# Performance work log

Measured on AMD Instinct MI355X. Metric: run time of the kernel, lower is better.

Reference implementation:

```python
import jax, jax.numpy as jnp
import numpy as np

EPS = float(np.finfo(np.float32).eps)  # matches torch.finfo(float32).eps
N_PTS, K_DIM, N_BINS = 1_000_000, 3, 21  # wv_tilde last dim = 2*N_BINS+1 = 43


def setup_inputs() -> dict:
    key = jax.random.key(0)
    k1, k2 = jax.random.split(key)
    # y in the open unit interval (points on the unit hypercube, per-coordinate)
    y = jax.random.uniform(k1, (N_PTS, K_DIM), jnp.float32, 1e-4, 1.0 - 1e-4)
    # network-predicted unnormalized widths/heights: [N, k, 2b+1]
    wv_tilde = jax.random.normal(k2, (N_PTS, K_DIM, 2 * N_BINS + 1), jnp.float32)
    return {"y": y, "wv_tilde": wv_tilde}


def _gather(t, idx):
    # gather along last axis with [..., 1] int index -> [...]
    return jnp.take_along_axis(t, idx, axis=-1)[..., 0]


def pwquad_flow(y, wv_tilde):
    """Faithful JAX port of ElementWisePWQuadraticTransform.flow (with jacobian)."""
    D = wv_tilde.shape[-1]
    nv = (D + 1) // 2                      # ceil(D/2) = b+1 vertex heights
    v_tilde = wv_tilde[..., :nv]           # [N,k,b+1]
    w_tilde = wv_tilde[..., nv:]           # [N,k,b]
    b = w_tilde.shape[-1]

    # normalized bin widths and their cumulative sums
    w = jnp.exp(w_tilde)
    wsum = jnp.cumsum(w, axis=-1)
    wnorm = wsum[..., -1:]
    w = w / wnorm
    wsum = wsum / wnorm
    zeros = jnp.zeros(wsum.shape[:-1] + (1,), wsum.dtype)
    wsum_shift = jnp.concatenate([zeros, wsum], axis=-1)   # [N,k,b+1]

    # modified softmax for vertex heights of the derivative (integrates to 1)
    ve = jnp.exp(v_tilde)
    trap = (ve[..., :-1] + ve[..., 1:]) * 0.5 * w          # trapezoid areas
    v = jnp.maximum(ve / trap.sum(-1, keepdims=True), 1e-6)  # [N,k,b+1]

    # cumulative CDF values at bin edges
    vw = jnp.concatenate(
        [zeros, jnp.cumsum((v[..., :-1] + v[..., 1:]) * 0.5 * w, axis=-1)],
        axis=-1)                                           # [N,k,b+1]

    # argmax-based bin search (identical to torch implementation)
    finder = jnp.where(vw > y[..., None], 0.0, 1.0)
    cat = jnp.concatenate([jnp.full_like(zeros, EPS), finder * (vw + 1.0)], axis=-1)
    mx = jnp.argmax(cat, axis=-1) - 1
    edges = jnp.clip(mx, 0, b - 1).astype(jnp.int32)[..., None]  # [N,k,1]

    v0 = _gather(v, edges)
    v1 = _gather(v, edges + 1)
    we = _gather(w, edges)

    # quadratic solve: (a/2) t^2 + bq t + c = 0  within the bin
    a = (v1 - v0) * we
    bq = v0 * we
    c = _gather(vw, edges) - y
    a = jnp.where(jnp.abs(a) < EPS, EPS, a)
    d = jnp.maximum(bq * bq - 2.0 * a * c, 0.0)
    sq = jnp.sqrt(d)
    sol1 = (-bq - sq) / a
    sol2 = (-bq + sq) / a
    sol = jnp.where((sol1 >= 0.0) & (sol1 < 1.0), sol1, sol2)
    sol = jnp.clip(sol, EPS, 1.0 - EPS)

    x = we * sol + _gather(wsum_shift, edges)
    x = jnp.clip(x, EPS, 1.0 - EPS)

    # log|det J| = -sum log(lerp(v0, v1, sol))
    logj = -jnp.sum(jnp.log(v0 + (v1 - v0) * sol), axis=-1, keepdims=True)
    return x, logj


def reference(y, wv_tilde):
    return pwquad_flow(y, wv_tilde)
```

## Files before the change

kernel.cpp:

```cpp
#include <hip/hip_runtime.h>
#include <math.h>

#define NROWS        3000000
#define ROWS_PER_BLK 192
#define NBINS        21
#define NV           22
#define DROW         43
#define FLOATS_PER_BLK (ROWS_PER_BLK * DROW)
#define F4_PER_BLK     (FLOATS_PER_BLK / 4)

__global__ __launch_bounds__(ROWS_PER_BLK) void pwquad_kernel(
    const float* __restrict__ y,
    const float* __restrict__ wv,
    float* __restrict__ out)
{
    __shared__ float lds[FLOATS_PER_BLK];
    __shared__ float lt[ROWS_PER_BLK];

    const int tid = threadIdx.x;
    const int blk = blockIdx.x;

    const float4* __restrict__ src4 =
        reinterpret_cast<const float4*>(wv + (long long)blk * FLOATS_PER_BLK);
    float4* l4 = reinterpret_cast<float4*>(lds);

    float4 r[10];
#pragma unroll
    for (int it = 0; it < 10; ++it) r[it] = src4[tid + it * ROWS_PER_BLK];
    const bool tail = (tid < (F4_PER_BLK - 10 * ROWS_PER_BLK));
    float4 rt;
    if (tail) rt = src4[tid + 10 * ROWS_PER_BLK];
#pragma unroll
    for (int it = 0; it < 10; ++it) l4[tid + it * ROWS_PER_BLK] = r[it];
    if (tail) l4[tid + 10 * ROWS_PER_BLK] = rt;
    __syncthreads();

    const int row = blk * ROWS_PER_BLK + tid;
    const float yv = y[row];
    const float* myrow = lds + tid * DROW;

    const float EPSF = 1.1920929e-07f;

    float w[NBINS];
    float wnorm = 0.f;
#pragma unroll
    for (int j = 0; j < NBINS; ++j) { w[j] = __expf(myrow[NV + j]); wnorm += w[j]; }
    const float invw = 1.0f / wnorm;
#pragma unroll
    for (int j = 0; j < NBINS; ++j) w[j] *= invw;

    float v[NV];
#pragma unroll
    for (int i = 0; i < NV; ++i) v[i] = __expf(myrow[i]);
    float T = 0.f;
#pragma unroll
    for (int j = 0; j < NBINS; ++j) T += (v[j] + v[j + 1]) * 0.5f * w[j];
    const float invT = 1.0f / T;
#pragma unroll
    for (int i = 0; i < NV; ++i) v[i] = fmaxf(v[i] * invT, 1e-6f);

    float vw = 0.f, wsum = 0.f;
    float vwe = 0.f, wse = 0.f;
    float v0 = v[0], v1 = v[1], we = w[0];
#pragma unroll
    for (int j = 0; j < 20; ++j) {
        const float inc = (v[j] + v[j + 1]) * 0.5f * w[j];
        vw += inc;
        wsum += w[j];
        const bool q = (vw <= yv);
        vwe = q ? vw       : vwe;
        wse = q ? wsum     : wse;
        v0  = q ? v[j + 1] : v0;
        v1  = q ? v[j + 2] : v1;
        we  = q ? w[j + 1] : we;
    }

    float a = (v1 - v0) * we;
    const float bq = v0 * we;
    const float c = vwe - yv;
    a = (fabsf(a) < EPSF) ? EPSF : a;
    const float dd = fmaxf(bq * bq - 2.0f * a * c, 0.f);
    const float sq = sqrtf(dd);
    const float sol1 = (-bq - sq) / a;
    const float sol2 = (-bq + sq) / a;
    float sol = (sol1 >= 0.f && sol1 < 1.f) ? sol1 : sol2;
    sol = fminf(fmaxf(sol, EPSF), 1.f - EPSF);
    float x = we * sol + wse;
    x = fminf(fmaxf(x, EPSF), 1.f - EPSF);
    out[row] = x;

    lt[tid] = __logf(v0 + (v1 - v0) * sol);
    __syncthreads();
    if (tid % 3 == 0) {
        out[NROWS + blk * (ROWS_PER_BLK / 3) + tid / 3] =
            -(lt[tid] + lt[tid + 1] + lt[tid + 2]);
    }
}

extern "C" void kernel_launch(void* const* d_in, const int* in_sizes, int n_in,
                              void* d_out, int out_size, void* d_ws, size_t ws_size,
                              hipStream_t stream) {
    const float* y  = (const float*)d_in[0];
    const float* wv = (const float*)d_in[1];
    float* out = (float*)d_out;

    const int nblocks = NROWS / ROWS_PER_BLK;
    pwquad_kernel<<<nblocks, ROWS_PER_BLK, 0, stream>>>(y, wv, out);
}
```

Baseline: 98.47 us.

## Load rows directly from global into registers, drop LDS staging and barriers

Replaces block-wide cooperative LDS staging of the 43-float rows with per-thread direct global loads of eleven unaligned 4-wide vectors, one wave handling 63 rows. The log-Jacobian reduction now uses wave shuffles instead of shared memory and a second barrier. This removes the LDS round-trip and both __syncthreads calls and allows higher occupancy. The cost is strided, non-coalesced per-thread loads (a 172-byte stride across lanes) and one idle lane per wave.

```diff
diff --git a/kernel.cpp b/kernel.cpp
--- a/kernel.cpp
+++ b/kernel.cpp
@@ -1,99 +1,103 @@
 #include <hip/hip_runtime.h>
 #include <math.h>
 
-#define NROWS        3000000
-#define ROWS_PER_BLK 192
-#define NBINS        21
-#define NV           22
-#define DROW         43
-#define FLOATS_PER_BLK (ROWS_PER_BLK * DROW)
-#define F4_PER_BLK     (FLOATS_PER_BLK / 4)
+#define NROWS    3000000
+#define NPTS     1000000
+#define NBINS    21
+#define NV       22
+#define DROW     43
+#define RPW      63
+#define NWAVES   ((NROWS + RPW - 1) / RPW)
+#define WPB      4
+#define NBLK     ((NWAVES + WPB - 1) / WPB)
 
-__global__ __launch_bounds__(ROWS_PER_BLK) void pwquad_kernel(
+typedef float f4a4 __attribute__((ext_vector_type(4), aligned(4)));
+
+__global__ __launch_bounds__(256, 4) void pwquad_kernel(
     const float* __restrict__ y,
     const float* __restrict__ wv,
     float* __restrict__ out)
 {
-    __shared__ float lds[FLOATS_PER_BLK];
-    __shared__ float lt[ROWS_PER_BLK];
-
-    const int tid = threadIdx.x;
-    const int blk = blockIdx.x;
-
-    const float4* __restrict__ src4 =
-        reinterpret_cast<const float4*>(wv + (long long)blk * FLOATS_PER_BLK);
-    float4* l4 = reinterpret_cast<float4*>(lds);
-
-    float4 r[10];
-#pragma unroll
-    for (int it = 0; it < 10; ++it) r[it] = src4[tid + it * ROWS_PER_BLK];
-    const bool tail = (tid < (F4_PER_BLK - 10 * ROWS_PER_BLK));
-    float4 rt;
-    if (tail) rt = src4[tid + 10 * ROWS_PER_BLK];
-#pragma unroll
-    for (int it = 0; it < 10; ++it) l4[tid + it * ROWS_PER_BLK] = r[it];
-    if (tail) l4[tid + 10 * ROWS_PER_BLK] = rt;
-    __syncthreads();
-
-    const int row = blk * ROWS_PER_BLK + tid;
-    const float yv = y[row];
-    const float* myrow = lds + tid * DROW;
-
+    const int lane = threadIdx.x & 63;
+    const int gw   = blockIdx.x * WPB + (threadIdx.x >> 6);
+    const int row  = gw * RPW + lane;
+    const bool active = (lane < RPW) && (row < NROWS);
     const float EPSF = 1.1920929e-07f;
 
-    float w[NBINS];
-    float wnorm = 0.f;
+    float ltv = 0.f;
+
+    if (active) {
+        const float* rp = wv + (size_t)row * DROW;
+        f4a4 r[11];
 #pragma unroll
-    for (int j = 0; j < NBINS; ++j) { w[j] = __expf(myrow[NV + j]); wnorm += w[j]; }
-    const float invw = 1.0f / wnorm;
+        for (int i = 0; i < 10; ++i)
+            r[i] = *reinterpret_cast<const f4a4*>(rp + 4 * i);
+        r[10] = *reinterpret_cast<const f4a4*>(rp + 39);
+
+        float in[43];
 #pragma unroll
-    for (int j = 0; j < NBINS; ++j) w[j] *= invw;
+        for (int i = 0; i < 10; ++i)
+#pragma unroll
+            for (int j = 0; j < 4; ++j) in[4 * i + j] = r[i][j];
+        in[40] = r[10][1]; in[41] = r[10][2]; in[42] = r[10][3];
 
-    float v[NV];
+        const float yv = y[row];
+
+        float w[NBINS];
+        float wnorm = 0.f;
 #pragma unroll
-    for (int i = 0; i < NV; ++i) v[i] = __expf(myrow[i]);
-    float T = 0.f;
+        for (int j = 0; j < NBINS; ++j) { w[j] = __expf(in[NV + j]); wnorm += w[j]; }
+        const float invw = 1.0f / wnorm;
 #pragma unroll
-    for (int j = 0; j < NBINS; ++j) T += (v[j] + v[j + 1]) * 0.5f * w[j];
-    const float invT = 1.0f / T;
+        for (int j = 0; j < NBINS; ++j) w[j] *= invw;
+
+        float v[NV];
 #pragma unroll
-    for (int i = 0; i < NV; ++i) v[i] = fmaxf(v[i] * invT, 1e-6f);
+        for (int i = 0; i < NV; ++i) v[i] = __expf(in[i]);
+        float T = 0.f;
+#pragma unroll
+        for (int j = 0; j < NBINS; ++j) T += (v[j] + v[j + 1]) * 0.5f * w[j];
+        const float invT = 1.0f / T;
+#pragma unroll
+        for (int i = 0; i < NV; ++i) v[i] = fmaxf(v[i] * invT, 1e-6f);
 
-    float vw = 0.f, wsum = 0.f;
-    float vwe = 0.f, wse = 0.f;
-    float v0 = v[0], v1 = v[1], we = w[0];
+        float vw = 0.f, wsum = 0.f;
+        float vwe = 0.f, wse = 0.f;
+        float v0 = v[0], v1 = v[1], we = w[0];
 #pragma unroll
-    for (int j = 0; j < 20; ++j) {
-        const float inc = (v[j] + v[j + 1]) * 0.5f * w[j];
-        vw += inc;
-        wsum += w[j];
-        const bool q = (vw <= yv);
-        vwe = q ? vw       : vwe;
-        wse = q ? wsum     : wse;
-        v0  = q ? v[j + 1] : v0;
-        v1  = q ? v[j + 2] : v1;
-        we  = q ? w[j + 1] : we;
+        for (int j = 0; j < 20; ++j) {
+            const float inc = (v[j] + v[j + 1]) * 0.5f * w[j];
+            vw += inc;
+            wsum += w[j];
+            const bool q = (vw <= yv);
+            vwe = q ? vw       : vwe;
+            wse = q ? wsum     : wse;
+            v0  = q ? v[j + 1] : v0;
+            v1  = q ? v[j + 2] : v1;
+            we  = q ? w[j + 1] : we;
+        }
+
+        float a = (v1 - v0) * we;
+        const float bq = v0 * we;
+        const float cc = vwe - yv;
+        a = (fabsf(a) < EPSF) ? EPSF : a;
+        const float dd = fmaxf(bq * bq - 2.0f * a * cc, 0.f);
+        const float sq = sqrtf(dd);
+        const float sol1 = (-bq - sq) / a;
+        const float sol2 = (-bq + sq) / a;
+        float sol = (sol1 >= 0.f && sol1 < 1.f) ? sol1 : sol2;
+        sol = fminf(fmaxf(sol, EPSF), 1.f - EPSF);
+        float x = we * sol + wse;
+        x = fminf(fmaxf(x, EPSF), 1.f - EPSF);
+
+        out[row] = x;
+        ltv = __logf(v0 + (v1 - v0) * sol);
     }
 
-    float a = (v1 - v0) * we;
-    const float bq = v0 * we;
-    const float c = vwe - yv;
-    a = (fabsf(a) < EPSF) ? EPSF : a;
-    const float dd = fmaxf(bq * bq - 2.0f * a * c, 0.f);
-    const float sq = sqrtf(dd);
-    const float sol1 = (-bq - sq) / a;
-    const float sol2 = (-bq + sq) / a;
-    float sol = (sol1 >= 0.f && sol1 < 1.f) ? sol1 : sol2;
-    sol = fminf(fmaxf(sol, EPSF), 1.f - EPSF);
-    float x = we * sol + wse;
-    x = fminf(fmaxf(x, EPSF), 1.f - EPSF);
-    out[row] = x;
-
-    lt[tid] = __logf(v0 + (v1 - v0) * sol);
-    __syncthreads();
-    if (tid % 3 == 0) {
-        out[NROWS + blk * (ROWS_PER_BLK / 3) + tid / 3] =
-            -(lt[tid] + lt[tid + 1] + lt[tid + 2]);
+    const float t1 = __shfl(ltv, (lane + 1) & 63);
+    const float t2 = __shfl(ltv, (lane + 2) & 63);
+    if (active && (lane % 3) == 0) {
+        out[NROWS + row / 3] = -(ltv + t1 + t2);
     }
 }
 
@@ -104,6 +108,5 @@
     const float* wv = (const float*)d_in[1];
     float* out = (float*)d_out;
 
-    const int nblocks = NROWS / ROWS_PER_BLK;
-    pwquad_kernel<<<nblocks, ROWS_PER_BLK, 0, stream>>>(y, wv, out);
+    pwquad_kernel<<<NBLK, 256, 0, stream>>>(y, wv, out);
 }
```

Result: slower. 110.9 us (+12.6%).
